# Performance work log

Measured on AMD Instinct MI355X. Metric: run time of the kernel, lower is better.

## Reference

```python
import jax, jax.numpy as jnp
import numpy as np

# Sizes from init_kwargs / input_specs
D_MODEL = 1024; D_INT = 64; KW = 32; B = 2; L = 4096
SAMPLING = np.array([5, 5, 2, 1, 1]); DILATIONS = np.array([1, 1, 2, 4, 8])
SUBHEADS = len(SAMPLING); HEADS = int(SAMPLING.sum())  # 5, 14
HEAD_OF_SUB = np.repeat(np.arange(SUBHEADS), SAMPLING)  # subhead index for each head
HEAD_DIL = np.repeat(DILATIONS, SAMPLING)                # dilation for each head


def _win_idx(dil):
    # centered dilated band, clipped at sequence edges -> [L, KW]
    offs = (np.arange(KW) - KW // 2) * dil
    return np.clip(np.arange(L)[:, None] + offs[None, :], 0, L - 1)

SUB_IDX = jnp.asarray(np.stack([_win_idx(d) for d in DILATIONS]))  # [SUBHEADS, L, KW]
HEAD_IDX = jnp.asarray(np.stack([_win_idx(d) for d in HEAD_DIL]))  # [HEADS, L, KW]


def setup_inputs() -> dict:
    rng = jax.random.key(0)
    ks = jax.random.split(rng, 9)
    n = lambda i, sh, sc=1.0: jax.random.normal(ks[i], sh, dtype=jnp.float32) * sc
    return dict(
        query=n(0, (B, L, D_MODEL)),
        key=n(1, (B, L, D_MODEL)),
        value=n(2, (B, L, D_MODEL)),
        Wq=n(3, (SUBHEADS, D_MODEL, D_INT), 0.02),
        bq=jnp.zeros((SUBHEADS, D_INT), jnp.float32),
        Wk=n(4, (SUBHEADS, D_MODEL, D_INT), 0.02),
        bk=jnp.zeros((SUBHEADS, D_INT), jnp.float32),
        Wv=n(5, (HEADS, D_MODEL, D_INT), 0.02),
        bv=jnp.zeros((HEADS, D_INT), jnp.float32),
        Ws=n(6, (HEADS, KW, KW), 0.05) + jnp.eye(KW, dtype=jnp.float32)[None],
        bs=jnp.zeros((HEADS, KW), jnp.float32),
        Wc=n(7, (HEADS * D_INT, D_MODEL), 0.02),
        bc=jnp.zeros((D_MODEL,), jnp.float32),
    )


def reference(query, key, value, Wq, bq, Wk, bk, Wv, bv, Ws, bs, Wc, bc):
    # per-subhead query/key projections: [S, B, L, Di]
    q = jnp.einsum('bld,sdi->sbli', query, Wq) + bq[:, None, None, :]
    k = jnp.einsum('bld,sdi->sbli', key, Wk) + bk[:, None, None, :]
    # per-head value projection: [H, B, L, Di]
    v = jnp.einsum('bld,hdi->hbli', value, Wv) + bv[:, None, None, :]
    # dilated banded key windows per subhead: [S, B, L, KW, Di]
    kw = jax.vmap(lambda kh, ix: kh[:, ix], in_axes=(0, 0))(k, SUB_IDX)
    # banded scores [S, B, L, KW]
    scores = jnp.einsum('sbli,sblki->sblk', q, kw) / jnp.sqrt(jnp.float32(D_INT))
    # supersample: replicate each subhead's scores to its heads -> [H, B, L, KW]
    scores_h = scores[HEAD_OF_SUB]
    # per-head positional supersampling linear on the score window
    sampled = jnp.einsum('hblk,hkm->hblm', scores_h, Ws) + bs[:, None, None, :]
    attn = jax.nn.softmax(sampled, axis=-1)
    # dilated value windows per head: [H, B, L, KW, Di]
    vw = jax.vmap(lambda vh, ix: vh[:, ix], in_axes=(0, 0))(v, HEAD_IDX)
    out = jnp.einsum('hblk,hblki->hbli', attn, vw)  # [H, B, L, Di]
    out = jnp.transpose(out, (1, 2, 0, 3)).reshape(B, L, HEADS * D_INT)
    return out @ Wc + bc  # [B, L, D_MODEL]
```

## Files before the change

kernel.cpp:

```cpp
#include <hip/hip_runtime.h>
#include <math.h>

#define D_MODEL 1024
#define D_INT   64
#define KW      32
#define L_SEQ   4096
#define SUBHEADS 5
#define HEADS   14
#define M_ROWS  8192
#define N_CAT   896
#define NQK     320
#define WMAX    312

typedef unsigned short us;
typedef unsigned int   uu;
typedef __attribute__((ext_vector_type(2))) unsigned int uu2;
typedef __attribute__((ext_vector_type(4))) unsigned int uu4;
typedef __attribute__((ext_vector_type(8))) short bf16x8_t;
typedef __attribute__((ext_vector_type(4))) float f32x4_t;

__device__ __forceinline__ float u2f(uu u) {
    float f; __builtin_memcpy(&f, &u, 4); return f;
}
__device__ __forceinline__ float blo(uu u) { return u2f(u << 16); }
__device__ __forceinline__ float bhi(uu u) { return u2f(u & 0xffff0000u); }
__device__ __forceinline__ us f2b(float f) {
    uu u; __builtin_memcpy(&u, &f, 4);
    u += 0x7fffu + ((u >> 16) & 1u);
    return (us)(u >> 16);
}
__device__ __forceinline__ void load16(void* lds, const void* g) {
    __builtin_amdgcn_global_load_lds(
        (const __attribute__((address_space(1))) unsigned int*)g,
        (__attribute__((address_space(3))) unsigned int*)lds, 16, 0, 0);
}
__device__ __forceinline__ int subhead_of(int h) {
    return (h < 5) ? 0 : (h < 10) ? 1 : (h < 12) ? 2 : (h == 12) ? 3 : 4;
}
__device__ __forceinline__ int dil_of_sub(int s) {
    return (s <= 1) ? 1 : (1 << (s - 1));
}

__global__ __launch_bounds__(256)
void cast3_bf16(const float4* __restrict__ s0, const float4* __restrict__ s1,
                const float4* __restrict__ s2, us* __restrict__ d0,
                us* __restrict__ d1, us* __restrict__ d2, int n4)
{
    int i = blockIdx.x * 256 + threadIdx.x;
    if (i >= n4) return;
    const float4* s = (blockIdx.y == 0) ? s0 : (blockIdx.y == 1) ? s1 : s2;
    us* d = (blockIdx.y == 0) ? d0 : (blockIdx.y == 1) ? d1 : d2;
    float4 v = s[i];
    ushort4 o;
    o.x = f2b(v.x); o.y = f2b(v.y); o.z = f2b(v.z); o.w = f2b(v.w);
    ((ushort4*)d)[i] = o;
}

__global__ __launch_bounds__(256)
void tcast(const float* __restrict__ s, us* __restrict__ d, int K, int N)
{
    __shared__ float t[32][33];
    const int b = blockIdx.z;
    const int k0 = blockIdx.x * 32, n0 = blockIdx.y * 32;
    const int tx = threadIdx.x & 31, ty = threadIdx.x >> 5;
#pragma unroll
    for (int r = 0; r < 32; r += 8)
        t[r + ty][tx] = s[((size_t)b * K + k0 + r + ty) * N + n0 + tx];
    __syncthreads();
#pragma unroll
    for (int r = 0; r < 32; r += 8)
        d[((size_t)b * N + n0 + r + ty) * K + k0 + tx] = f2b(t[tx][r + ty]);
}

__global__ __launch_bounds__(256)
void gemm_bf16(const us* __restrict__ A, const us* __restrict__ Bt,
               const float* __restrict__ bias, void* __restrict__ Cv,
               int K, int ldC, int outBf16)
{
    __shared__ us As[128 * 64];
    __shared__ us Bs[64 * 64];
    const int row0 = blockIdx.x << 7, col0 = blockIdx.y << 6;
    const int tid = threadIdx.x, w = tid >> 6, lane = tid & 63;
    const int m = lane & 15, quad = lane >> 4;
    const int sr = lane >> 3;
    const int scs = (lane & 7) ^ sr;

    f32x4_t z = {0.f, 0.f, 0.f, 0.f};
    f32x4_t acc[2][4] = {{z, z, z, z}, {z, z, z, z}};

    for (int k0 = 0; k0 < K; k0 += 64) {
#pragma unroll
        for (int p = 0; p < 4; p++) {
            const int r = w * 32 + p * 8 + sr;
            load16(&As[(w * 32 + p * 8) * 64], A + (size_t)(row0 + r) * K + k0 + scs * 8);
        }
#pragma unroll
        for (int p = 0; p < 2; p++) {
            const int r = w * 16 + p * 8 + sr;
            load16(&Bs[(w * 16 + p * 8) * 64], Bt + (size_t)(col0 + r) * K + k0 + scs * 8);
        }
        __syncthreads();
#pragma unroll
        for (int ks = 0; ks < 2; ks++) {
            const int slot = ((ks * 4 + quad) ^ (m & 7)) * 8;
            bf16x8_t a0 = *(const bf16x8_t*)&As[(w * 32 + m) * 64 + slot];
            bf16x8_t a1 = *(const bf16x8_t*)&As[(w * 32 + 16 + m) * 64 + slot];
#pragma unroll
            for (int t = 0; t < 4; t++) {
                bf16x8_t bb = *(const bf16x8_t*)&Bs[(t * 16 + m) * 64 + slot];
                acc[0][t] = __builtin_amdgcn_mfma_f32_16x16x32_bf16(a0, bb, acc[0][t], 0, 0, 0);
                acc[1][t] = __builtin_amdgcn_mfma_f32_16x16x32_bf16(a1, bb, acc[1][t], 0, 0, 0);
            }
        }
        __syncthreads();
    }

#pragma unroll
    for (int tm = 0; tm < 2; tm++) {
        const int rbase = row0 + w * 32 + tm * 16 + quad * 4;
        if (outBf16) {
            us* Cb = (us*)Cv;
#pragma unroll
            for (int t = 0; t < 4; t++) {
                const int col = col0 + t * 16 + m;
                const float bi = bias[col];
#pragma unroll
                for (int r = 0; r < 4; r++)
                    Cb[(size_t)(rbase + r) * ldC + col] = f2b(acc[tm][t][r] + bi);
            }
        } else {
            float* Cb = (float*)Cv;
#pragma unroll
            for (int t = 0; t < 4; t++) {
                const int col = col0 + t * 16 + m;
                const float bi = bias[col];
#pragma unroll
                for (int r = 0; r < 4; r++)
                    Cb[(size_t)(rbase + r) * ldC + col] = acc[tm][t][r] + bi;
            }
        }
    }
}

__global__ __launch_bounds__(256)
void gemm_bf16_128(const us* __restrict__ A, const us* __restrict__ Bt,
                   const float* __restrict__ bias, void* __restrict__ Cv,
                   int K, int ldC, int outBf16)
{
    __shared__ us As[128 * 64];
    __shared__ us Bs[128 * 64];
    const int row0 = blockIdx.x << 7, col0 = blockIdx.y << 7;
    const int tid = threadIdx.x, w = tid >> 6, lane = tid & 63;
    const int m = lane & 15, quad = lane >> 4;
    const int sr = lane >> 3;
    const int scs = (lane & 7) ^ sr;
    const int mrow0 = (w & 1) * 64, ncol0 = (w >> 1) * 64;

    f32x4_t z = {0.f, 0.f, 0.f, 0.f};
    f32x4_t acc[4][4] = {{z,z,z,z},{z,z,z,z},{z,z,z,z},{z,z,z,z}};

    for (int k0 = 0; k0 < K; k0 += 64) {
#pragma unroll
        for (int p = 0; p < 4; p++) {
            const int r = w * 32 + p * 8 + sr;
            load16(&As[(w * 32 + p * 8) * 64], A  + (size_t)(row0 + r) * K + k0 + scs * 8);
            load16(&Bs[(w * 32 + p * 8) * 64], Bt + (size_t)(col0 + r) * K + k0 + scs * 8);
        }
        __syncthreads();
#pragma unroll
        for (int ks = 0; ks < 2; ks++) {
            const int slot = ((ks * 4 + quad) ^ (m & 7)) * 8;
            bf16x8_t a[4], b[4];
#pragma unroll
            for (int t = 0; t < 4; t++) {
                a[t] = *(const bf16x8_t*)&As[(mrow0 + t * 16 + m) * 64 + slot];
                b[t] = *(const bf16x8_t*)&Bs[(ncol0 + t * 16 + m) * 64 + slot];
            }
#pragma unroll
            for (int i = 0; i < 4; i++)
#pragma unroll
                for (int j = 0; j < 4; j++)
                    acc[i][j] = __builtin_amdgcn_mfma_f32_16x16x32_bf16(a[i], b[j], acc[i][j], 0, 0, 0);
        }
        __syncthreads();
    }

#pragma unroll
    for (int i = 0; i < 4; i++) {
        const int rbase = row0 + mrow0 + i * 16 + quad * 4;
        if (outBf16) {
            us* Cb = (us*)Cv;
#pragma unroll
            for (int j = 0; j < 4; j++) {
                const int col = col0 + ncol0 + j * 16 + m;
                const float bi = bias[col];
#pragma unroll
                for (int r = 0; r < 4; r++)
                    Cb[(size_t)(rbase + r) * ldC + col] = f2b(acc[i][j][r] + bi);
            }
        } else {
            float* Cb = (float*)Cv;
#pragma unroll
            for (int j = 0; j < 4; j++) {
                const int col = col0 + ncol0 + j * 16 + m;
                const float bi = bias[col];
#pragma unroll
                for (int r = 0; r < 4; r++)
                    Cb[(size_t)(rbase + r) * ldC + col] = acc[i][j][r] + bi;
            }
        }
    }
}

__global__ __launch_bounds__(256)
void score_kernel(const us* __restrict__ qb, const us* __restrict__ kb,
                  float* __restrict__ scores)
{
    __shared__ uu kslab[WMAX * 36];
    __shared__ uu qslab[64 * 32];

    const int tid  = threadIdx.x;
    const int wave = tid >> 6;
    const int lane = tid & 63;
    const int j    = lane & 31;
    const int half = lane >> 5;
    const int s    = blockIdx.y;
    const int d    = dil_of_sub(s);
    const int ml0  = blockIdx.x * 64;
    const int l0   = ml0 & 4095;
    const int bm   = ml0 - l0;
    const int W    = 64 + 31 * d;

    const uu* kg = (const uu*)kb;
    const uu* qg = (const uu*)qb;

    for (int idx = tid; idx < W * 32; idx += 256) {
        int r = idx >> 5, c = idx & 31;
        int src = l0 - 16 * d + r;
        src = src < 0 ? 0 : (src > 4095 ? 4095 : src);
        kslab[r * 36 + c] = kg[(size_t)(bm + src) * 160 + s * 32 + c];
    }
    for (int idx = tid; idx < 64 * 32; idx += 256) {
        int r = idx >> 5, c = idx & 31;
        qslab[r * 32 + c] = qg[(size_t)(ml0 + r) * 160 + s * 32 + c];
    }
    __syncthreads();

#pragma unroll
    for (int i = 0; i < 8; i++) {
        const int p = wave * 16 + i * 2 + half;
        const uu4* k4 = (const uu4*)&kslab[(p + j * d) * 36];
        const uu4* q4 = (const uu4*)&qslab[p * 32];
        float acc = 0.f;
#pragma unroll
        for (int q = 0; q < 8; q++) {
            uu4 kd = k4[q];
            uu4 qd = q4[q];
#pragma unroll
            for (int u = 0; u < 4; u++) {
                acc = fmaf(blo(kd[u]), blo(qd[u]), acc);
                acc = fmaf(bhi(kd[u]), bhi(qd[u]), acc);
            }
        }
        scores[((size_t)s * M_ROWS + ml0 + p) * 32 + j] = acc * 0.125f;
    }
}

__global__ __launch_bounds__(256)
void head_kernel(const float* __restrict__ scores, const us* __restrict__ vb,
                 const float* __restrict__ Ws, const float* __restrict__ bs,
                 us* __restrict__ ab)
{
    __shared__ uu    vslab[WMAX * 34];
    __shared__ float scb[64 * 32];
    __shared__ float atb[64 * 32];

    const int tid  = threadIdx.x;
    const int wave = tid >> 6;
    const int lane = tid & 63;
    const int j    = lane & 31;
    const int half = lane >> 5;
    const int h    = blockIdx.y;
    const int s    = subhead_of(h);
    const int d    = dil_of_sub(s);
    const int ml0  = blockIdx.x * 64;
    const int l0   = ml0 & 4095;
    const int bm   = ml0 - l0;
    const int W    = 64 + 31 * d;

    const uu* vg = (const uu*)vb;
    for (int idx = tid; idx < W * 32; idx += 256) {
        int r = idx >> 5, c = idx & 31;
        int src = l0 - 16 * d + r;
        src = src < 0 ? 0 : (src > 4095 ? 4095 : src);
        vslab[r * 34 + c] = vg[(size_t)(bm + src) * 448 + h * 32 + c];
    }
#pragma unroll
    for (int t = 0; t < 8; t++) {
        int idx = t * 256 + tid;
        scb[idx] = scores[((size_t)s * M_ROWS + ml0) * 32 + idx];
    }

    float wsr[32];
#pragma unroll
    for (int k = 0; k < 32; k++) wsr[k] = Ws[(size_t)h * 1024 + k * 32 + j];
    const float bsv = bs[h * 32 + j];
    __syncthreads();

#pragma unroll
    for (int i = 0; i < 8; i++) {
        const int p = wave * 16 + i * 2 + half;
        const float4* s4 = (const float4*)&scb[p * 32];
        float acc = bsv;
#pragma unroll
        for (int q = 0; q < 8; q++) {
            float4 v = s4[q];
            acc = fmaf(v.x, wsr[q * 4 + 0], acc);
            acc = fmaf(v.y, wsr[q * 4 + 1], acc);
            acc = fmaf(v.z, wsr[q * 4 + 2], acc);
            acc = fmaf(v.w, wsr[q * 4 + 3], acc);
        }
        float mx = acc;
#pragma unroll
        for (int off = 16; off > 0; off >>= 1) mx = fmaxf(mx, __shfl_xor(mx, off, 64));
        float ex = __expf(acc - mx);
        float sum = ex;
#pragma unroll
        for (int off = 16; off > 0; off >>= 1) sum += __shfl_xor(sum, off, 64);
        atb[p * 32 + j] = ex / sum;
    }

    const int pp = lane >> 4;
    const int cq = lane & 15;
#pragma unroll
    for (int g = 0; g < 4; g++) {
        const int p  = wave * 16 + g * 4 + pp;
        const int ml = ml0 + p;
        const float4* a4 = (const float4*)&atb[p * 32];
        float o0 = 0.f, o1 = 0.f, o2 = 0.f, o3 = 0.f;
#pragma unroll
        for (int q = 0; q < 8; q++) {
            float4 a = a4[q];
#pragma unroll
            for (int u = 0; u < 4; u++) {
                const int mm = q * 4 + u;
                uu2 vd = *(const uu2*)&vslab[(p + mm * d) * 34 + cq * 2];
                const float av = (u == 0) ? a.x : (u == 1) ? a.y : (u == 2) ? a.z : a.w;
                o0 = fmaf(blo(vd.x), av, o0);
                o1 = fmaf(bhi(vd.x), av, o1);
                o2 = fmaf(blo(vd.y), av, o2);
                o3 = fmaf(bhi(vd.y), av, o3);
            }
        }
        uu2 od;
        od.x = (uu)f2b(o0) | ((uu)f2b(o1) << 16);
        od.y = (uu)f2b(o2) | ((uu)f2b(o3) << 16);
        *(uu2*)&((uu*)ab)[(size_t)ml * 448 + h * 32 + cq * 2] = od;
    }
}

extern "C" void kernel_launch(void* const* d_in, const int* in_sizes, int n_in,
                              void* d_out, int out_size, void* d_ws, size_t ws_size,
                              hipStream_t stream)
{
    const float* query = (const float*)d_in[0];
    const float* key   = (const float*)d_in[1];
    const float* value = (const float*)d_in[2];
    const float* Wq    = (const float*)d_in[3];
    const float* bq    = (const float*)d_in[4];
    const float* Wk    = (const float*)d_in[5];
    const float* bk    = (const float*)d_in[6];
    const float* Wv    = (const float*)d_in[7];
    const float* bv    = (const float*)d_in[8];
    const float* Ws    = (const float*)d_in[9];
    const float* bs    = (const float*)d_in[10];
    const float* Wc    = (const float*)d_in[11];
    const float* bc    = (const float*)d_in[12];
    float* out = (float*)d_out;

    us* w = (us*)d_ws;
    us* Xq  = w;
    us* ab  = w;
    us* Xk  = Xq  + (size_t)M_ROWS * D_MODEL;
    float* scores = (float*)Xk;
    us* Xv  = Xk  + (size_t)M_ROWS * D_MODEL;
    us* Wqt = Xv  + (size_t)M_ROWS * D_MODEL;
    us* Wkt = Wqt + (size_t)SUBHEADS * D_INT * D_MODEL;
    us* Wvt = Wkt + (size_t)SUBHEADS * D_INT * D_MODEL;
    us* Wct = Wvt + (size_t)HEADS * D_INT * D_MODEL;
    us* qbuf = Wct + (size_t)D_MODEL * N_CAT;
    us* kbuf = qbuf + (size_t)M_ROWS * NQK;
    us* vbuf = kbuf + (size_t)M_ROWS * NQK;

    const int n4 = M_ROWS * D_MODEL / 4;
    cast3_bf16<<<dim3(n4 / 256, 3), dim3(256), 0, stream>>>(
        (const float4*)query, (const float4*)key, (const float4*)value,
        Xq, Xk, Xv, n4);

    tcast<<<dim3(D_MODEL / 32, D_INT / 32, SUBHEADS), dim3(256), 0, stream>>>(Wq, Wqt, D_MODEL, D_INT);
    tcast<<<dim3(D_MODEL / 32, D_INT / 32, SUBHEADS), dim3(256), 0, stream>>>(Wk, Wkt, D_MODEL, D_INT);
    tcast<<<dim3(D_MODEL / 32, D_INT / 32, HEADS),    dim3(256), 0, stream>>>(Wv, Wvt, D_MODEL, D_INT);
    tcast<<<dim3(N_CAT / 32, D_MODEL / 32, 1),        dim3(256), 0, stream>>>(Wc, Wct, N_CAT, D_MODEL);

    dim3 blk(256);
    gemm_bf16<<<dim3(M_ROWS / 128, NQK / 64), blk, 0, stream>>>(
        Xq, Wqt, bq, qbuf, D_MODEL, NQK, 1);
    gemm_bf16<<<dim3(M_ROWS / 128, NQK / 64), blk, 0, stream>>>(
        Xk, Wkt, bk, kbuf, D_MODEL, NQK, 1);
    gemm_bf16_128<<<dim3(M_ROWS / 128, N_CAT / 128), blk, 0, stream>>>(
        Xv, Wvt, bv, vbuf, D_MODEL, N_CAT, 1);

    score_kernel<<<dim3(M_ROWS / 64, SUBHEADS), blk, 0, stream>>>(qbuf, kbuf, scores);
    head_kernel<<<dim3(M_ROWS / 64, HEADS), blk, 0, stream>>>(scores, vbuf, Ws, bs, ab);

    gemm_bf16_128<<<dim3(M_ROWS / 128, D_MODEL / 128), blk, 0, stream>>>(
        ab, Wct, bc, out, N_CAT, D_MODEL, 0);
}
```

Measured before the change: 301.5 us.

## Merge prep kernels, fuse QK GEMMs, specialize LDS size per dilation, vectorize head output

Folds the input casts and four weight transposes into one prep kernel, and merges the Q and K projection GEMMs into a single launch along a z dimension, cutting launch count. Score and head kernels are templated on the LDS slab size, so small-dilation subheads use a smaller slab, which can raise occupancy. The head kernel reuses one shared buffer for scores and attention weights, and its value accumulation now has each lane produce 8 outputs with 128-bit LDS loads and stores. Costs are more kernel variants and a larger register footprint in the head kernel.

```diff
diff --git a/kernel.cpp b/kernel.cpp
--- a/kernel.cpp
+++ b/kernel.cpp
@@ -10,11 +10,9 @@
 #define M_ROWS  8192
 #define N_CAT   896
 #define NQK     320
-#define WMAX    312
 
 typedef unsigned short us;
 typedef unsigned int   uu;
-typedef __attribute__((ext_vector_type(2))) unsigned int uu2;
 typedef __attribute__((ext_vector_type(4))) unsigned int uu4;
 typedef __attribute__((ext_vector_type(8))) short bf16x8_t;
 typedef __attribute__((ext_vector_type(4))) float f32x4_t;
@@ -29,6 +27,9 @@
     u += 0x7fffu + ((u >> 16) & 1u);
     return (us)(u >> 16);
 }
+__device__ __forceinline__ uu pack2(float a, float b) {
+    return (uu)f2b(a) | ((uu)f2b(b) << 16);
+}
 __device__ __forceinline__ void load16(void* lds, const void* g) {
     __builtin_amdgcn_global_load_lds(
         (const __attribute__((address_space(1))) unsigned int*)g,
@@ -41,52 +42,72 @@
     return (s <= 1) ? 1 : (1 << (s - 1));
 }
 
+#define CAST_BLK 24576
 __global__ __launch_bounds__(256)
-void cast3_bf16(const float4* __restrict__ s0, const float4* __restrict__ s1,
-                const float4* __restrict__ s2, us* __restrict__ d0,
-                us* __restrict__ d1, us* __restrict__ d2, int n4)
-{
-    int i = blockIdx.x * 256 + threadIdx.x;
-    if (i >= n4) return;
-    const float4* s = (blockIdx.y == 0) ? s0 : (blockIdx.y == 1) ? s1 : s2;
-    us* d = (blockIdx.y == 0) ? d0 : (blockIdx.y == 1) ? d1 : d2;
-    float4 v = s[i];
-    ushort4 o;
-    o.x = f2b(v.x); o.y = f2b(v.y); o.z = f2b(v.z); o.w = f2b(v.w);
-    ((ushort4*)d)[i] = o;
-}
-
-__global__ __launch_bounds__(256)
-void tcast(const float* __restrict__ s, us* __restrict__ d, int K, int N)
+void prep_kernel(const float4* __restrict__ q, const float4* __restrict__ k,
+                 const float4* __restrict__ v,
+                 const float* __restrict__ Wq, const float* __restrict__ Wk,
+                 const float* __restrict__ Wv, const float* __restrict__ Wc,
+                 us* __restrict__ Xq, us* __restrict__ Xk, us* __restrict__ Xv,
+                 us* __restrict__ Wqt, us* __restrict__ Wkt,
+                 us* __restrict__ Wvt, us* __restrict__ Wct)
 {
     __shared__ float t[32][33];
-    const int b = blockIdx.z;
-    const int k0 = blockIdx.x * 32, n0 = blockIdx.y * 32;
-    const int tx = threadIdx.x & 31, ty = threadIdx.x >> 5;
+    const int b = blockIdx.x, tid = threadIdx.x;
+
+    if (b < CAST_BLK) {
+        const int which = b >> 13;
+        const int i = ((b & 8191) << 8) + tid;
+        const float4* s = (which == 0) ? q : (which == 1) ? k : v;
+        us* d = (which == 0) ? Xq : (which == 1) ? Xk : Xv;
+        float4 x = s[i];
+        ushort4 o;
+        o.x = f2b(x.x); o.y = f2b(x.y); o.z = f2b(x.z); o.w = f2b(x.w);
+        ((ushort4*)d)[i] = o;
+        return;
+    }
+
+    int g = b - CAST_BLK;
+    const float* S; us* D; int K, N;
+    if (g < 640) {
+        if (g < 320) { S = Wq; D = Wqt; } else { S = Wk; D = Wkt; g -= 320; }
+        K = 1024; N = 64;
+    } else if (g < 1536) {
+        g -= 640; S = Wv; D = Wvt; K = 1024; N = 64;
+    } else {
+        g -= 1536; S = Wc; D = Wct; K = 896; N = 1024;
+    }
+    const int nkx = K >> 5;
+    const int kx = g % nkx;
+    const int rest = g / nkx;
+    const int ny = rest % (N >> 5);
+    const int z  = rest / (N >> 5);
+    const int k0 = kx * 32, n0 = ny * 32;
+    S += (size_t)z * K * N;
+    D += (size_t)z * K * N;
+    const int tx = tid & 31, ty = tid >> 5;
 #pragma unroll
     for (int r = 0; r < 32; r += 8)
-        t[r + ty][tx] = s[((size_t)b * K + k0 + r + ty) * N + n0 + tx];
+        t[r + ty][tx] = S[(size_t)(k0 + r + ty) * N + n0 + tx];
     __syncthreads();
 #pragma unroll
     for (int r = 0; r < 32; r += 8)
-        d[((size_t)b * N + n0 + r + ty) * K + k0 + tx] = f2b(t[tx][r + ty]);
-}
-
-__global__ __launch_bounds__(256)
-void gemm_bf16(const us* __restrict__ A, const us* __restrict__ Bt,
-               const float* __restrict__ bias, void* __restrict__ Cv,
-               int K, int ldC, int outBf16)
-{
-    __shared__ us As[128 * 64];
-    __shared__ us Bs[64 * 64];
+        D[(size_t)(n0 + r + ty) * K + k0 + tx] = f2b(t[tx][r + ty]);
+}
+
+__device__ __forceinline__
+void gemm64_core(const us* __restrict__ A, const us* __restrict__ Bt,
+                 const float* __restrict__ bias, us* __restrict__ C,
+                 int K, int ldC, us* As, us* Bs)
+{
     const int row0 = blockIdx.x << 7, col0 = blockIdx.y << 6;
     const int tid = threadIdx.x, w = tid >> 6, lane = tid & 63;
     const int m = lane & 15, quad = lane >> 4;
     const int sr = lane >> 3;
     const int scs = (lane & 7) ^ sr;
 
-    f32x4_t z = {0.f, 0.f, 0.f, 0.f};
-    f32x4_t acc[2][4] = {{z, z, z, z}, {z, z, z, z}};
+    f32x4_t z4 = {0.f, 0.f, 0.f, 0.f};
+    f32x4_t acc[2][4] = {{z4, z4, z4, z4}, {z4, z4, z4, z4}};
 
     for (int k0 = 0; k0 < K; k0 += 64) {
 #pragma unroll
@@ -118,28 +139,28 @@
 #pragma unroll
     for (int tm = 0; tm < 2; tm++) {
         const int rbase = row0 + w * 32 + tm * 16 + quad * 4;
-        if (outBf16) {
-            us* Cb = (us*)Cv;
-#pragma unroll
-            for (int t = 0; t < 4; t++) {
-                const int col = col0 + t * 16 + m;
-                const float bi = bias[col];
-#pragma unroll
-                for (int r = 0; r < 4; r++)
-                    Cb[(size_t)(rbase + r) * ldC + col] = f2b(acc[tm][t][r] + bi);
-            }
-        } else {
-            float* Cb = (float*)Cv;
-#pragma unroll
-            for (int t = 0; t < 4; t++) {
-                const int col = col0 + t * 16 + m;
-                const float bi = bias[col];
-#pragma unroll
-                for (int r = 0; r < 4; r++)
-                    Cb[(size_t)(rbase + r) * ldC + col] = acc[tm][t][r] + bi;
-            }
-        }
-    }
+#pragma unroll
+        for (int t = 0; t < 4; t++) {
+            const int col = col0 + t * 16 + m;
+            const float bi = bias[col];
+#pragma unroll
+            for (int r = 0; r < 4; r++)
+                C[(size_t)(rbase + r) * ldC + col] = f2b(acc[tm][t][r] + bi);
+        }
+    }
+}
+
+__global__ __launch_bounds__(256)
+void gemm_qk(const us* __restrict__ Xq, const us* __restrict__ Xk,
+             const us* __restrict__ Wqt, const us* __restrict__ Wkt,
+             const float* __restrict__ bq, const float* __restrict__ bk,
+             us* __restrict__ qbuf, us* __restrict__ kbuf)
+{
+    __shared__ us As[128 * 64];
+    __shared__ us Bs[64 * 64];
+    const int z = blockIdx.z;
+    gemm64_core(z ? Xk : Xq, z ? Wkt : Wqt, z ? bk : bq, z ? kbuf : qbuf,
+                D_MODEL, NQK, As, Bs);
 }
 
 __global__ __launch_bounds__(256)
@@ -212,11 +233,12 @@
     }
 }
 
+template<int ROWS>
 __global__ __launch_bounds__(256)
 void score_kernel(const us* __restrict__ qb, const us* __restrict__ kb,
-                  float* __restrict__ scores)
-{
-    __shared__ uu kslab[WMAX * 36];
+                  float* __restrict__ scores, int sbase)
+{
+    __shared__ uu kslab[ROWS * 36];
     __shared__ uu qslab[64 * 32];
 
     const int tid  = threadIdx.x;
@@ -224,7 +246,7 @@
     const int lane = tid & 63;
     const int j    = lane & 31;
     const int half = lane >> 5;
-    const int s    = blockIdx.y;
+    const int s    = sbase + blockIdx.y;
     const int d    = dil_of_sub(s);
     const int ml0  = blockIdx.x * 64;
     const int l0   = ml0 & 4095;
@@ -256,31 +278,30 @@
         for (int q = 0; q < 8; q++) {
             uu4 kd = k4[q];
             uu4 qd = q4[q];
-#pragma unroll
-            for (int u = 0; u < 4; u++) {
-                acc = fmaf(blo(kd[u]), blo(qd[u]), acc);
-                acc = fmaf(bhi(kd[u]), bhi(qd[u]), acc);
-            }
+            acc = fmaf(blo(kd.x), blo(qd.x), acc); acc = fmaf(bhi(kd.x), bhi(qd.x), acc);
+            acc = fmaf(blo(kd.y), blo(qd.y), acc); acc = fmaf(bhi(kd.y), bhi(qd.y), acc);
+            acc = fmaf(blo(kd.z), blo(qd.z), acc); acc = fmaf(bhi(kd.z), bhi(qd.z), acc);
+            acc = fmaf(blo(kd.w), blo(qd.w), acc); acc = fmaf(bhi(kd.w), bhi(qd.w), acc);
         }
         scores[((size_t)s * M_ROWS + ml0 + p) * 32 + j] = acc * 0.125f;
     }
 }
 
+template<int ROWS>
 __global__ __launch_bounds__(256)
 void head_kernel(const float* __restrict__ scores, const us* __restrict__ vb,
                  const float* __restrict__ Ws, const float* __restrict__ bs,
-                 us* __restrict__ ab)
-{
-    __shared__ uu    vslab[WMAX * 34];
-    __shared__ float scb[64 * 32];
-    __shared__ float atb[64 * 32];
+                 us* __restrict__ ab, int hbase)
+{
+    __shared__ uu    vslab[ROWS * 36];
+    __shared__ float sab[64 * 36];
 
     const int tid  = threadIdx.x;
     const int wave = tid >> 6;
     const int lane = tid & 63;
     const int j    = lane & 31;
     const int half = lane >> 5;
-    const int h    = blockIdx.y;
+    const int h    = hbase + blockIdx.y;
     const int s    = subhead_of(h);
     const int d    = dil_of_sub(s);
     const int ml0  = blockIdx.x * 64;
@@ -293,14 +314,17 @@
         int r = idx >> 5, c = idx & 31;
         int src = l0 - 16 * d + r;
         src = src < 0 ? 0 : (src > 4095 ? 4095 : src);
-        vslab[r * 34 + c] = vg[(size_t)(bm + src) * 448 + h * 32 + c];
-    }
-#pragma unroll
-    for (int t = 0; t < 8; t++) {
-        int idx = t * 256 + tid;
-        scb[idx] = scores[((size_t)s * M_ROWS + ml0) * 32 + idx];
-    }
-
+        vslab[r * 36 + c] = vg[(size_t)(bm + src) * 448 + h * 32 + c];
+    }
+    {
+        const float4* g4 = (const float4*)(scores + ((size_t)s * M_ROWS + ml0) * 32);
+#pragma unroll
+        for (int t = 0; t < 2; t++) {
+            int i4 = t * 256 + tid;
+            int r = i4 >> 3, c4 = i4 & 7;
+            *(float4*)&sab[r * 36 + c4 * 4] = g4[i4];
+        }
+    }
     float wsr[32];
 #pragma unroll
     for (int k = 0; k < 32; k++) wsr[k] = Ws[(size_t)h * 1024 + k * 32 + j];
@@ -310,7 +334,7 @@
 #pragma unroll
     for (int i = 0; i < 8; i++) {
         const int p = wave * 16 + i * 2 + half;
-        const float4* s4 = (const float4*)&scb[p * 32];
+        const float4* s4 = (const float4*)&sab[p * 36];
         float acc = bsv;
 #pragma unroll
         for (int q = 0; q < 8; q++) {
@@ -327,35 +351,30 @@
         float sum = ex;
 #pragma unroll
         for (int off = 16; off > 0; off >>= 1) sum += __shfl_xor(sum, off, 64);
-        atb[p * 32 + j] = ex / sum;
-    }
-
-    const int pp = lane >> 4;
-    const int cq = lane & 15;
-#pragma unroll
-    for (int g = 0; g < 4; g++) {
-        const int p  = wave * 16 + g * 4 + pp;
+        sab[p * 36 + j] = ex / sum;
+    }
+
+    const int o = lane >> 3;
+    const int c = lane & 7;
+#pragma unroll
+    for (int pass = 0; pass < 2; pass++) {
+        const int p  = wave * 16 + pass * 8 + o;
         const int ml = ml0 + p;
-        const float4* a4 = (const float4*)&atb[p * 32];
-        float o0 = 0.f, o1 = 0.f, o2 = 0.f, o3 = 0.f;
-#pragma unroll
-        for (int q = 0; q < 8; q++) {
-            float4 a = a4[q];
-#pragma unroll
-            for (int u = 0; u < 4; u++) {
-                const int mm = q * 4 + u;
-                uu2 vd = *(const uu2*)&vslab[(p + mm * d) * 34 + cq * 2];
-                const float av = (u == 0) ? a.x : (u == 1) ? a.y : (u == 2) ? a.z : a.w;
-                o0 = fmaf(blo(vd.x), av, o0);
-                o1 = fmaf(bhi(vd.x), av, o1);
-                o2 = fmaf(blo(vd.y), av, o2);
-                o3 = fmaf(bhi(vd.y), av, o3);
-            }
-        }
-        uu2 od;
-        od.x = (uu)f2b(o0) | ((uu)f2b(o1) << 16);
-        od.y = (uu)f2b(o2) | ((uu)f2b(o3) << 16);
-        *(uu2*)&((uu*)ab)[(size_t)ml * 448 + h * 32 + cq * 2] = od;
+        float a0 = 0.f, a1 = 0.f, a2 = 0.f, a3 = 0.f;
+        float a4 = 0.f, a5 = 0.f, a6 = 0.f, a7 = 0.f;
+#pragma unroll
+        for (int mm = 0; mm < 32; mm++) {
+            const float at = sab[p * 36 + mm];
+            uu4 vd = *(const uu4*)&vslab[(p + mm * d) * 36 + c * 4];
+            a0 = fmaf(blo(vd.x), at, a0); a1 = fmaf(bhi(vd.x), at, a1);
+            a2 = fmaf(blo(vd.y), at, a2); a3 = fmaf(bhi(vd.y), at, a3);
+            a4 = fmaf(blo(vd.z), at, a4); a5 = fmaf(bhi(vd.z), at, a5);
+            a6 = fmaf(blo(vd.w), at, a6); a7 = fmaf(bhi(vd.w), at, a7);
+        }
+        uu4 od;
+        od.x = pack2(a0, a1); od.y = pack2(a2, a3);
+        od.z = pack2(a4, a5); od.w = pack2(a6, a7);
+        *(uu4*)&((uu*)ab)[(size_t)ml * 448 + h * 32 + c * 4] = od;
     }
 }
 
@@ -392,26 +411,23 @@
     us* kbuf = qbuf + (size_t)M_ROWS * NQK;
     us* vbuf = kbuf + (size_t)M_ROWS * NQK;
 
-    const int n4 = M_ROWS * D_MODEL / 4;
-    cast3_bf16<<<dim3(n4 / 256, 3), dim3(256), 0, stream>>>(
+    dim3 blk(256);
+
+    prep_kernel<<<dim3(CAST_BLK + 2432), blk, 0, stream>>>(
         (const float4*)query, (const float4*)key, (const float4*)value,
-        Xq, Xk, Xv, n4);
-
-    tcast<<<dim3(D_MODEL / 32, D_INT / 32, SUBHEADS), dim3(256), 0, stream>>>(Wq, Wqt, D_MODEL, D_INT);
-    tcast<<<dim3(D_MODEL / 32, D_INT / 32, SUBHEADS), dim3(256), 0, stream>>>(Wk, Wkt, D_MODEL, D_INT);
-    tcast<<<dim3(D_MODEL / 32, D_INT / 32, HEADS),    dim3(256), 0, stream>>>(Wv, Wvt, D_MODEL, D_INT);
-    tcast<<<dim3(N_CAT / 32, D_MODEL / 32, 1),        dim3(256), 0, stream>>>(Wc, Wct, N_CAT, D_MODEL);
-
-    dim3 blk(256);
-    gemm_bf16<<<dim3(M_ROWS / 128, NQK / 64), blk, 0, stream>>>(
-        Xq, Wqt, bq, qbuf, D_MODEL, NQK, 1);
-    gemm_bf16<<<dim3(M_ROWS / 128, NQK / 64), blk, 0, stream>>>(
-        Xk, Wkt, bk, kbuf, D_MODEL, NQK, 1);
+        Wq, Wk, Wv, Wc, Xq, Xk, Xv, Wqt, Wkt, Wvt, Wct);
+
+    gemm_qk<<<dim3(M_ROWS / 128, NQK / 64, 2), blk, 0, stream>>>(
+        Xq, Xk, Wqt, Wkt, bq, bk, qbuf, kbuf);
+
     gemm_bf16_128<<<dim3(M_ROWS / 128, N_CAT / 128), blk, 0, stream>>>(
         Xv, Wvt, bv, vbuf, D_MODEL, N_CAT, 1);
 
-    score_kernel<<<dim3(M_ROWS / 64, SUBHEADS), blk, 0, stream>>>(qbuf, kbuf, scores);
-    head_kernel<<<dim3(M_ROWS / 64, HEADS), blk, 0, stream>>>(scores, vbuf, Ws, bs, ab);
+    score_kernel<126><<<dim3(M_ROWS / 64, 3), blk, 0, stream>>>(qbuf, kbuf, scores, 0);
+    score_kernel<312><<<dim3(M_ROWS / 64, 2), blk, 0, stream>>>(qbuf, kbuf, scores, 3);
+
+    head_kernel<312><<<dim3(M_ROWS / 64, 2),  blk, 0, stream>>>(scores, vbuf, Ws, bs, ab, 12);
+    head_kernel<126><<<dim3(M_ROWS / 64, 12), blk, 0, stream>>>(scores, vbuf, Ws, bs, ab, 0);
 
     gemm_bf16_128<<<dim3(M_ROWS / 128, D_MODEL / 128), blk, 0, stream>>>(
         ab, Wct, bc, out, N_CAT, D_MODEL, 0);
```

Result: faster. 284.9 us (-5.5%).
